# Kernel tuning notes

Hardware: AMD Instinct MI355X
Metric: run time of the kernel (lower is better)

## Reference

```python
import jax, jax.numpy as jnp
import numpy as np

B, L, H = 32, 512, 1024
Q = 128
VA_H = 256

def setup_inputs() -> dict:
    key = jax.random.key(0)
    ks = jax.random.split(key, 12)
    hidden_states = jax.random.normal(ks[0], (B, L, H), dtype=jnp.float32)
    # Build valid inclusive spans: start in [2, L-16), length in [0, 8)
    asp_s = jax.random.randint(ks[1], (B, Q), 2, L - 16)
    asp_e = asp_s + jax.random.randint(ks[2], (B, Q), 0, 8)
    opi_s = jax.random.randint(ks[3], (B, Q), 2, L - 16)
    opi_e = opi_s + jax.random.randint(ks[4], (B, Q), 0, 8)
    null = jax.random.uniform(ks[5], (B, Q)) < 0.1
    asp_s = jnp.where(null, 0, asp_s)
    quad_spans = jnp.stack([asp_s, asp_e, opi_s, opi_e], axis=-1).astype(jnp.int64)
    quad_mask = (jax.random.uniform(ks[6], (B, Q)) > 0.3).astype(jnp.float32)
    # MLP params (torch Linear: y = x @ W.T + b), kaiming-ish scale
    def lin(k, out_d, in_d):
        return jax.random.normal(k, (out_d, in_d), dtype=jnp.float32) / np.sqrt(in_d)
    W1 = lin(ks[7], VA_H, 3 * H); b1 = jnp.zeros((VA_H,), jnp.float32)
    W2 = lin(ks[8], VA_H // 2, VA_H); b2 = jnp.zeros((VA_H // 2,), jnp.float32)
    W3 = lin(ks[9], 2, VA_H // 2); b3 = jnp.zeros((2,), jnp.float32)
    return {"hidden_states": hidden_states, "quad_spans": quad_spans,
            "quad_mask": quad_mask, "W1": W1, "b1": b1, "W2": W2, "b2": b2,
            "W3": W3, "b3": b3}

def _pool_spans(hidden_states, s, e):
    # hidden_states: [B,L,H]; s,e: [B,Q] inclusive indices
    pos = jnp.arange(hidden_states.shape[1])  # [L]
    valid = (s >= 2) & (e >= s)               # [B,Q]
    m = (pos[None, None, :] >= s[..., None]) & (pos[None, None, :] <= e[..., None])
    m = (m & valid[..., None]).astype(hidden_states.dtype)  # [B,Q,L]
    cnt = jnp.maximum(m.sum(-1, keepdims=True), 1.0)        # [B,Q,1]
    mean = jnp.einsum('bql,blh->bqh', m, hidden_states) / cnt
    sep = hidden_states[:, 1:2, :]                           # [B,1,H] fallback
    return jnp.where(valid[..., None], mean, sep)

def reference(hidden_states, quad_spans, quad_mask, W1, b1, W2, b2, W3, b3):
    h_asp = _pool_spans(hidden_states, quad_spans[..., 0], quad_spans[..., 1])
    h_opi = _pool_spans(hidden_states, quad_spans[..., 2], quad_spans[..., 3])
    h_pair = jnp.concatenate([h_asp, h_opi, h_asp * h_opi], axis=-1)  # [B,Q,3H]
    x = jax.nn.gelu(h_pair @ W1.T + b1, approximate=False)  # torch GELU = erf
    x = jax.nn.gelu(x @ W2.T + b2, approximate=False)
    va = jax.nn.sigmoid(x @ W3.T + b3) * 8.0 + 1.0          # [B,Q,2] in [1,9]
    # Invalid pairs stay zero, matching the torch loop's skipped entries
    return va * (quad_mask >= 0.5).astype(va.dtype)[..., None]
```

## Files before the change

kernel.cpp:

```cpp
#include <hip/hip_runtime.h>
#include <hip/hip_bf16.h>
#include <math.h>

typedef __bf16 bf16x8 __attribute__((ext_vector_type(8)));
typedef float f32x4 __attribute__((ext_vector_type(4)));

__device__ __forceinline__ unsigned short f2bf(float x) {
    union { float f; unsigned int u; } v; v.f = x;
    unsigned int r = v.u + 0x7fffu + ((v.u >> 16) & 1u);
    return (unsigned short)(r >> 16);
}
__device__ __forceinline__ float gelu_exact(float v) {
    return 0.5f * v * (1.0f + erff(v * 0.70710678118654752f));
}

__global__ __launch_bounds__(256) void prep_kernel(const float* __restrict__ hs,
                                                   const int* __restrict__ spans,
                                                   const float* __restrict__ W1,
                                                   unsigned short* __restrict__ hp,
                                                   unsigned short* __restrict__ w1b,
                                                   float* __restrict__ xacc1) {
    const int blk = blockIdx.x;
    const int tid = threadIdx.x;

    if (blk >= 4096) {
        if (blk < 4864) {
            const int i = (blk - 4096) * 256 + tid;
            float4 f = ((const float4*)W1)[i];
            ushort4 u;
            u.x = f2bf(f.x); u.y = f2bf(f.y); u.z = f2bf(f.z); u.w = f2bf(f.w);
            ((ushort4*)w1b)[i] = u;
        } else {
            const int i = (blk - 4864) * 256 + tid;
            ((float4*)xacc1)[i] = make_float4(0.f, 0.f, 0.f, 0.f);
        }
        return;
    }

    const int pair = blk;
    const int b = pair >> 7;

    const bool is64 = (spans[1] == 0);
    int s_a, e_a, s_o, e_o;
    if (is64) {
        s_a = spans[(pair * 4 + 0) * 2]; e_a = spans[(pair * 4 + 1) * 2];
        s_o = spans[(pair * 4 + 2) * 2]; e_o = spans[(pair * 4 + 3) * 2];
    } else {
        s_a = spans[pair * 4 + 0]; e_a = spans[pair * 4 + 1];
        s_o = spans[pair * 4 + 2]; e_o = spans[pair * 4 + 3];
    }

    const float4* base = (const float4*)hs + (size_t)b * 512 * 256;

    float4 A, O;
    if (s_a >= 2 && e_a >= s_a) {
        float sx = 0.f, sy = 0.f, sz = 0.f, sw = 0.f;
        for (int t = s_a; t <= e_a; ++t) {
            float4 v = base[t * 256 + tid];
            sx += v.x; sy += v.y; sz += v.z; sw += v.w;
        }
        float inv = 1.0f / (float)(e_a - s_a + 1);
        A.x = sx * inv; A.y = sy * inv; A.z = sz * inv; A.w = sw * inv;
    } else {
        A = base[256 + tid];
    }
    if (s_o >= 2 && e_o >= s_o) {
        float sx = 0.f, sy = 0.f, sz = 0.f, sw = 0.f;
        for (int t = s_o; t <= e_o; ++t) {
            float4 v = base[t * 256 + tid];
            sx += v.x; sy += v.y; sz += v.z; sw += v.w;
        }
        float inv = 1.0f / (float)(e_o - s_o + 1);
        O.x = sx * inv; O.y = sy * inv; O.z = sz * inv; O.w = sw * inv;
    } else {
        O = base[256 + tid];
    }

    unsigned short* row = hp + (size_t)pair * 3072;
    const int d = tid * 4;
    ushort4 pa, po, pp;
    pa.x = f2bf(A.x); pa.y = f2bf(A.y); pa.z = f2bf(A.z); pa.w = f2bf(A.w);
    po.x = f2bf(O.x); po.y = f2bf(O.y); po.z = f2bf(O.z); po.w = f2bf(O.w);
    pp.x = f2bf(A.x * O.x); pp.y = f2bf(A.y * O.y);
    pp.z = f2bf(A.z * O.z); pp.w = f2bf(A.w * O.w);
    *(ushort4*)(row + d) = pa;
    *(ushort4*)(row + 1024 + d) = po;
    *(ushort4*)(row + 2048 + d) = pp;
}

__global__ __launch_bounds__(256, 4) void gemm1_mfma(const unsigned short* __restrict__ A,
                                                     const unsigned short* __restrict__ Bw,
                                                     float* __restrict__ xacc) {
    __shared__ __align__(16) unsigned short As[128 * 64];
    __shared__ __align__(16) unsigned short Bs[64 * 64];

    const int tid = threadIdx.x;
    const int lane = tid & 63;
    const int wid = tid >> 6;
    const int quad = lane >> 4;
    const int l16 = lane & 15;
    const int wM = wid * 32;
    const int m0 = blockIdx.x * 128;
    const int n0 = blockIdx.y * 64;
    const int kb = blockIdx.z * 384;

    const int srow = tid >> 3;
    const int lchunk = (tid & 7) ^ (srow & 7);
    const unsigned short* Abase = A + (size_t)(m0 + srow) * 3072 + kb + lchunk * 8;
    const unsigned short* Bbase = Bw + (size_t)(n0 + srow) * 3072 + kb + lchunk * 8;

    int aoff[2][2], boff[4][2];
#pragma unroll
    for (int h = 0; h < 2; ++h) {
#pragma unroll
        for (int mi = 0; mi < 2; ++mi) {
            const int row = wM + mi * 16 + l16;
            const int pc = (h * 4 + quad) ^ (row & 7);
            aoff[mi][h] = row * 64 + pc * 8;
        }
#pragma unroll
        for (int ni = 0; ni < 4; ++ni) {
            const int row = ni * 16 + l16;
            const int pc = (h * 4 + quad) ^ (row & 7);
            boff[ni][h] = row * 64 + pc * 8;
        }
    }

    f32x4 acc[2][4] = {};

#pragma unroll
    for (int it = 0; it < 6; ++it) {
        const int kadv = it * 64;
#pragma unroll
        for (int j = 0; j < 4; ++j) {
            __builtin_amdgcn_global_load_lds(
                (const __attribute__((address_space(1))) void*)(Abase + (size_t)j * 32 * 3072 + kadv),
                (__attribute__((address_space(3))) void*)(&As[(j * 256 + tid) * 8]),
                16, 0, 0);
        }
#pragma unroll
        for (int j = 0; j < 2; ++j) {
            __builtin_amdgcn_global_load_lds(
                (const __attribute__((address_space(1))) void*)(Bbase + (size_t)j * 32 * 3072 + kadv),
                (__attribute__((address_space(3))) void*)(&Bs[(j * 256 + tid) * 8]),
                16, 0, 0);
        }
        __syncthreads();
#pragma unroll
        for (int h = 0; h < 2; ++h) {
            bf16x8 af[2], bfr[4];
#pragma unroll
            for (int mi = 0; mi < 2; ++mi) af[mi] = *(const bf16x8*)&As[aoff[mi][h]];
#pragma unroll
            for (int ni = 0; ni < 4; ++ni) bfr[ni] = *(const bf16x8*)&Bs[boff[ni][h]];
#pragma unroll
            for (int mi = 0; mi < 2; ++mi)
#pragma unroll
                for (int ni = 0; ni < 4; ++ni)
                    acc[mi][ni] = __builtin_amdgcn_mfma_f32_16x16x32_bf16(
                        af[mi], bfr[ni], acc[mi][ni], 0, 0, 0);
        }
        __syncthreads();
    }

#pragma unroll
    for (int mi = 0; mi < 2; ++mi) {
#pragma unroll
        for (int ni = 0; ni < 4; ++ni) {
            const int n = n0 + ni * 16 + l16;
#pragma unroll
            for (int rr = 0; rr < 4; ++rr) {
                const int m = m0 + wM + mi * 16 + quad * 4 + rr;
                unsafeAtomicAdd(&xacc[(size_t)m * 256 + n], acc[mi][ni][rr]);
            }
        }
    }
}

__global__ __launch_bounds__(256) void mlp2g_head(const float* __restrict__ xacc,
                                                  const float* __restrict__ b1,
                                                  const float* __restrict__ W2f,
                                                  const float* __restrict__ b2,
                                                  const float* __restrict__ W3,
                                                  const float* __restrict__ b3,
                                                  const float* __restrict__ mask,
                                                  float* __restrict__ out) {
    __shared__ __align__(16) unsigned short Xs[32][72];
    __shared__ __align__(16) unsigned short Ws[128][72];
    __shared__ float X2[32][132];

    const int tid = threadIdx.x;
    const int lane = tid & 63;
    const int wid = tid >> 6;
    const int wM = (wid >> 1) * 16;
    const int wN = (wid & 1) * 64;
    const int quad = lane >> 4;
    const int l16 = lane & 15;
    const int m0 = blockIdx.x * 32;

    f32x4 acc[4] = {};

    for (int k0 = 0; k0 < 256; k0 += 64) {
        {
            const int r = tid >> 3, c = (tid & 7) * 8;
            const float* src = xacc + (size_t)(m0 + r) * 256 + k0 + c;
            float4 f0 = *(const float4*)src;
            float4 f1 = *(const float4*)(src + 4);
            float4 g0 = *(const float4*)(b1 + k0 + c);
            float4 g1 = *(const float4*)(b1 + k0 + c + 4);
            ushort4 u0, u1;
            u0.x = f2bf(gelu_exact(f0.x + g0.x)); u0.y = f2bf(gelu_exact(f0.y + g0.y));
            u0.z = f2bf(gelu_exact(f0.z + g0.z)); u0.w = f2bf(gelu_exact(f0.w + g0.w));
            u1.x = f2bf(gelu_exact(f1.x + g1.x)); u1.y = f2bf(gelu_exact(f1.y + g1.y));
            u1.z = f2bf(gelu_exact(f1.z + g1.z)); u1.w = f2bf(gelu_exact(f1.w + g1.w));
            *(ushort4*)&Xs[r][c] = u0;
            *(ushort4*)&Xs[r][c + 4] = u1;
        }
#pragma unroll
        for (int p = 0; p < 4; ++p) {
            const int v = tid + p * 256;
            const int r = v >> 3, c = (v & 7) * 8;
            const float* src = W2f + (size_t)r * 256 + k0 + c;
            float4 f0 = *(const float4*)src;
            float4 f1 = *(const float4*)(src + 4);
            ushort4 u;
            u.x = f2bf(f0.x); u.y = f2bf(f0.y); u.z = f2bf(f0.z); u.w = f2bf(f0.w);
            *(ushort4*)&Ws[r][c] = u;
            u.x = f2bf(f1.x); u.y = f2bf(f1.y); u.z = f2bf(f1.z); u.w = f2bf(f1.w);
            *(ushort4*)&Ws[r][c + 4] = u;
        }
        __syncthreads();
#pragma unroll
        for (int kk = 0; kk < 64; kk += 32) {
            bf16x8 a = *(const bf16x8*)&Xs[wM + l16][kk + quad * 8];
#pragma unroll
            for (int ni = 0; ni < 4; ++ni) {
                bf16x8 b = *(const bf16x8*)&Ws[wN + ni * 16 + l16][kk + quad * 8];
                acc[ni] = __builtin_amdgcn_mfma_f32_16x16x32_bf16(a, b, acc[ni], 0, 0, 0);
            }
        }
        __syncthreads();
    }

#pragma unroll
    for (int ni = 0; ni < 4; ++ni) {
        const int n = wN + ni * 16 + l16;
        const float bn = b2[n];
#pragma unroll
        for (int rr = 0; rr < 4; ++rr) {
            const int m = wM + quad * 4 + rr;
            X2[m][n] = gelu_exact(acc[ni][rr] + bn);
        }
    }
    __syncthreads();

    const int p = tid >> 3;
    const int cc = (tid & 7) * 16;
    float a0 = 0.f, a1 = 0.f;
#pragma unroll
    for (int j = 0; j < 16; ++j) {
        const float xv = X2[p][cc + j];
        a0 += xv * W3[cc + j];
        a1 += xv * W3[128 + cc + j];
    }
    a0 += __shfl_xor(a0, 1); a0 += __shfl_xor(a0, 2); a0 += __shfl_xor(a0, 4);
    a1 += __shfl_xor(a1, 1); a1 += __shfl_xor(a1, 2); a1 += __shfl_xor(a1, 4);
    if ((tid & 7) == 0) {
        const int pair = m0 + p;
        const float mk = (mask[pair] >= 0.5f) ? 1.0f : 0.0f;
        out[pair * 2 + 0] = ((1.0f / (1.0f + expf(-(a0 + b3[0])))) * 8.0f + 1.0f) * mk;
        out[pair * 2 + 1] = ((1.0f / (1.0f + expf(-(a1 + b3[1])))) * 8.0f + 1.0f) * mk;
    }
}

extern "C" void kernel_launch(void* const* d_in, const int* in_sizes, int n_in,
                              void* d_out, int out_size, void* d_ws, size_t ws_size,
                              hipStream_t stream) {
    const float* hs   = (const float*)d_in[0];
    const int*   spans= (const int*)d_in[1];
    const float* mask = (const float*)d_in[2];
    const float* W1   = (const float*)d_in[3];
    const float* b1   = (const float*)d_in[4];
    const float* W2   = (const float*)d_in[5];
    const float* b2   = (const float*)d_in[6];
    const float* W3   = (const float*)d_in[7];
    const float* b3   = (const float*)d_in[8];
    float* out = (float*)d_out;

    unsigned short* hp    = (unsigned short*)d_ws;
    float*          xacc1 = (float*)((char*)d_ws + 25165824);
    unsigned short* w1b   = (unsigned short*)((char*)d_ws + 29360128);

    prep_kernel<<<dim3(5888), dim3(256), 0, stream>>>(hs, spans, W1, hp, w1b, xacc1);
    gemm1_mfma<<<dim3(32, 4, 8), dim3(256), 0, stream>>>(hp, w1b, xacc1);
    mlp2g_head<<<dim3(128), dim3(256), 0, stream>>>(xacc1, b1, W2, b2, W3, b3, mask, out);
}
```

Baseline: 161.3 us.

## Fuse GEMM1, MLP layer 2 and head into one double-buffered kernel

Replaces the split-K GEMM1 with its atomic accumulation buffer, and the separate MLP2/head kernel, with a single kernel. Each block owns 16 rows and computes all 256 hidden columns over the full K=3072, using double-buffered LDS tiles. GELU, layer 2 and the head then run on-chip, which removes the xacc zeroing, the atomics and one launch. The cost is only 256 blocks, each streaming the whole W1 (about 1.5MB) through a single K loop. That gives lower parallelism and a much larger total W1 read volume, mostly served from L2.

```diff
diff --git a/kernel.cpp b/kernel.cpp
--- a/kernel.cpp
+++ b/kernel.cpp
@@ -10,6 +10,10 @@
     unsigned int r = v.u + 0x7fffu + ((v.u >> 16) & 1u);
     return (unsigned short)(r >> 16);
 }
+__device__ __forceinline__ float bf2f(unsigned short h) {
+    union { unsigned int u; float f; } v; v.u = ((unsigned int)h) << 16;
+    return v.f;
+}
 __device__ __forceinline__ float gelu_exact(float v) {
     return 0.5f * v * (1.0f + erff(v * 0.70710678118654752f));
 }
@@ -18,22 +22,16 @@
                                                    const int* __restrict__ spans,
                                                    const float* __restrict__ W1,
                                                    unsigned short* __restrict__ hp,
-                                                   unsigned short* __restrict__ w1b,
-                                                   float* __restrict__ xacc1) {
+                                                   unsigned short* __restrict__ w1b) {
     const int blk = blockIdx.x;
     const int tid = threadIdx.x;
 
     if (blk >= 4096) {
-        if (blk < 4864) {
-            const int i = (blk - 4096) * 256 + tid;
-            float4 f = ((const float4*)W1)[i];
-            ushort4 u;
-            u.x = f2bf(f.x); u.y = f2bf(f.y); u.z = f2bf(f.z); u.w = f2bf(f.w);
-            ((ushort4*)w1b)[i] = u;
-        } else {
-            const int i = (blk - 4864) * 256 + tid;
-            ((float4*)xacc1)[i] = make_float4(0.f, 0.f, 0.f, 0.f);
-        }
+        const int i = (blk - 4096) * 256 + tid;
+        float4 f = ((const float4*)W1)[i];
+        ushort4 u;
+        u.x = f2bf(f.x); u.y = f2bf(f.y); u.z = f2bf(f.z); u.w = f2bf(f.w);
+        ((ushort4*)w1b)[i] = u;
         return;
     }
 
@@ -88,184 +86,160 @@
     *(ushort4*)(row + 2048 + d) = pp;
 }
 
-__global__ __launch_bounds__(256, 4) void gemm1_mfma(const unsigned short* __restrict__ A,
-                                                     const unsigned short* __restrict__ Bw,
-                                                     float* __restrict__ xacc) {
-    __shared__ __align__(16) unsigned short As[128 * 64];
-    __shared__ __align__(16) unsigned short Bs[64 * 64];
+__global__ __launch_bounds__(256) void mlp_all(const unsigned short* __restrict__ hp,
+                                               const unsigned short* __restrict__ w1b,
+                                               const float* __restrict__ b1,
+                                               const float* __restrict__ W2f,
+                                               const float* __restrict__ b2,
+                                               const float* __restrict__ W3,
+                                               const float* __restrict__ b3,
+                                               const float* __restrict__ mask,
+                                               float* __restrict__ out) {
+    __shared__ __align__(16) unsigned char smem[84480];
+    unsigned short* Ab0 = (unsigned short*)smem;
+    unsigned short* Ab1 = (unsigned short*)(smem + 2048);
+    unsigned short* Bb0 = (unsigned short*)(smem + 4096);
+    unsigned short* Bb1 = (unsigned short*)(smem + 36864);
+    unsigned short* x1s = (unsigned short*)smem;
+    unsigned short* w2s = (unsigned short*)(smem + 8448);
+    float*          x2s = (float*)(smem + 76032);
 
     const int tid = threadIdx.x;
     const int lane = tid & 63;
     const int wid = tid >> 6;
     const int quad = lane >> 4;
     const int l16 = lane & 15;
-    const int wM = wid * 32;
-    const int m0 = blockIdx.x * 128;
-    const int n0 = blockIdx.y * 64;
-    const int kb = blockIdx.z * 384;
+    const int m0 = blockIdx.x * 16;
 
     const int srow = tid >> 3;
-    const int lchunk = (tid & 7) ^ (srow & 7);
-    const unsigned short* Abase = A + (size_t)(m0 + srow) * 3072 + kb + lchunk * 8;
-    const unsigned short* Bbase = Bw + (size_t)(n0 + srow) * 3072 + kb + lchunk * 8;
-
-    int aoff[2][2], boff[4][2];
+    const int lch = (tid & 7) ^ (srow & 7);
+    const unsigned short* Aptr = hp + (size_t)(m0 + srow) * 3072 + lch * 8;
+    const unsigned short* Bptr = w1b + (size_t)srow * 3072 + lch * 8;
+
+    int aoff[2], boff[4][2];
 #pragma unroll
     for (int h = 0; h < 2; ++h) {
-#pragma unroll
-        for (int mi = 0; mi < 2; ++mi) {
-            const int row = wM + mi * 16 + l16;
-            const int pc = (h * 4 + quad) ^ (row & 7);
-            aoff[mi][h] = row * 64 + pc * 8;
+        {
+            const int pc = (h * 4 + quad) ^ (l16 & 7);
+            aoff[h] = l16 * 64 + pc * 8;
         }
 #pragma unroll
         for (int ni = 0; ni < 4; ++ni) {
-            const int row = ni * 16 + l16;
+            const int row = wid * 64 + ni * 16 + l16;
             const int pc = (h * 4 + quad) ^ (row & 7);
             boff[ni][h] = row * 64 + pc * 8;
         }
     }
 
-    f32x4 acc[2][4] = {};
-
-#pragma unroll
-    for (int it = 0; it < 6; ++it) {
-        const int kadv = it * 64;
-#pragma unroll
-        for (int j = 0; j < 4; ++j) {
-            __builtin_amdgcn_global_load_lds(
-                (const __attribute__((address_space(1))) void*)(Abase + (size_t)j * 32 * 3072 + kadv),
-                (__attribute__((address_space(3))) void*)(&As[(j * 256 + tid) * 8]),
-                16, 0, 0);
-        }
-#pragma unroll
-        for (int j = 0; j < 2; ++j) {
-            __builtin_amdgcn_global_load_lds(
-                (const __attribute__((address_space(1))) void*)(Bbase + (size_t)j * 32 * 3072 + kadv),
-                (__attribute__((address_space(3))) void*)(&Bs[(j * 256 + tid) * 8]),
-                16, 0, 0);
-        }
+    f32x4 acc[4] = {};
+
+    if (tid < 128)
+        __builtin_amdgcn_global_load_lds(
+            (const __attribute__((address_space(1))) void*)Aptr,
+            (__attribute__((address_space(3))) void*)(Ab0 + tid * 8), 16, 0, 0);
+#pragma unroll
+    for (int j = 0; j < 8; ++j)
+        __builtin_amdgcn_global_load_lds(
+            (const __attribute__((address_space(1))) void*)(Bptr + (size_t)j * 32 * 3072),
+            (__attribute__((address_space(3))) void*)(Bb0 + (j * 256 + tid) * 8), 16, 0, 0);
+
+    for (int it = 0; it < 48; ++it) {
+        unsigned short* Ac = (it & 1) ? Ab1 : Ab0;
+        unsigned short* Bc = (it & 1) ? Bb1 : Bb0;
         __syncthreads();
+        if (it + 1 < 48) {
+            unsigned short* An = (it & 1) ? Ab0 : Ab1;
+            unsigned short* Bn = (it & 1) ? Bb0 : Bb1;
+            const int kadv = (it + 1) * 64;
+            if (tid < 128)
+                __builtin_amdgcn_global_load_lds(
+                    (const __attribute__((address_space(1))) void*)(Aptr + kadv),
+                    (__attribute__((address_space(3))) void*)(An + tid * 8), 16, 0, 0);
+#pragma unroll
+            for (int j = 0; j < 8; ++j)
+                __builtin_amdgcn_global_load_lds(
+                    (const __attribute__((address_space(1))) void*)(Bptr + (size_t)j * 32 * 3072 + kadv),
+                    (__attribute__((address_space(3))) void*)(Bn + (j * 256 + tid) * 8), 16, 0, 0);
+        }
 #pragma unroll
         for (int h = 0; h < 2; ++h) {
-            bf16x8 af[2], bfr[4];
-#pragma unroll
-            for (int mi = 0; mi < 2; ++mi) af[mi] = *(const bf16x8*)&As[aoff[mi][h]];
-#pragma unroll
-            for (int ni = 0; ni < 4; ++ni) bfr[ni] = *(const bf16x8*)&Bs[boff[ni][h]];
-#pragma unroll
-            for (int mi = 0; mi < 2; ++mi)
-#pragma unroll
-                for (int ni = 0; ni < 4; ++ni)
-                    acc[mi][ni] = __builtin_amdgcn_mfma_f32_16x16x32_bf16(
-                        af[mi], bfr[ni], acc[mi][ni], 0, 0, 0);
-        }
-        __syncthreads();
-    }
-
-#pragma unroll
-    for (int mi = 0; mi < 2; ++mi) {
-#pragma unroll
-        for (int ni = 0; ni < 4; ++ni) {
-            const int n = n0 + ni * 16 + l16;
-#pragma unroll
-            for (int rr = 0; rr < 4; ++rr) {
-                const int m = m0 + wM + mi * 16 + quad * 4 + rr;
-                unsafeAtomicAdd(&xacc[(size_t)m * 256 + n], acc[mi][ni][rr]);
-            }
-        }
-    }
-}
-
-__global__ __launch_bounds__(256) void mlp2g_head(const float* __restrict__ xacc,
-                                                  const float* __restrict__ b1,
-                                                  const float* __restrict__ W2f,
-                                                  const float* __restrict__ b2,
-                                                  const float* __restrict__ W3,
-                                                  const float* __restrict__ b3,
-                                                  const float* __restrict__ mask,
-                                                  float* __restrict__ out) {
-    __shared__ __align__(16) unsigned short Xs[32][72];
-    __shared__ __align__(16) unsigned short Ws[128][72];
-    __shared__ float X2[32][132];
-
-    const int tid = threadIdx.x;
-    const int lane = tid & 63;
-    const int wid = tid >> 6;
-    const int wM = (wid >> 1) * 16;
-    const int wN = (wid & 1) * 64;
-    const int quad = lane >> 4;
-    const int l16 = lane & 15;
-    const int m0 = blockIdx.x * 32;
-
-    f32x4 acc[4] = {};
-
-    for (int k0 = 0; k0 < 256; k0 += 64) {
-        {
-            const int r = tid >> 3, c = (tid & 7) * 8;
-            const float* src = xacc + (size_t)(m0 + r) * 256 + k0 + c;
-            float4 f0 = *(const float4*)src;
-            float4 f1 = *(const float4*)(src + 4);
-            float4 g0 = *(const float4*)(b1 + k0 + c);
-            float4 g1 = *(const float4*)(b1 + k0 + c + 4);
-            ushort4 u0, u1;
-            u0.x = f2bf(gelu_exact(f0.x + g0.x)); u0.y = f2bf(gelu_exact(f0.y + g0.y));
-            u0.z = f2bf(gelu_exact(f0.z + g0.z)); u0.w = f2bf(gelu_exact(f0.w + g0.w));
-            u1.x = f2bf(gelu_exact(f1.x + g1.x)); u1.y = f2bf(gelu_exact(f1.y + g1.y));
-            u1.z = f2bf(gelu_exact(f1.z + g1.z)); u1.w = f2bf(gelu_exact(f1.w + g1.w));
-            *(ushort4*)&Xs[r][c] = u0;
-            *(ushort4*)&Xs[r][c + 4] = u1;
-        }
-#pragma unroll
-        for (int p = 0; p < 4; ++p) {
-            const int v = tid + p * 256;
-            const int r = v >> 3, c = (v & 7) * 8;
-            const float* src = W2f + (size_t)r * 256 + k0 + c;
-            float4 f0 = *(const float4*)src;
-            float4 f1 = *(const float4*)(src + 4);
-            ushort4 u;
-            u.x = f2bf(f0.x); u.y = f2bf(f0.y); u.z = f2bf(f0.z); u.w = f2bf(f0.w);
-            *(ushort4*)&Ws[r][c] = u;
-            u.x = f2bf(f1.x); u.y = f2bf(f1.y); u.z = f2bf(f1.z); u.w = f2bf(f1.w);
-            *(ushort4*)&Ws[r][c + 4] = u;
-        }
-        __syncthreads();
-#pragma unroll
-        for (int kk = 0; kk < 64; kk += 32) {
-            bf16x8 a = *(const bf16x8*)&Xs[wM + l16][kk + quad * 8];
+            bf16x8 a = *(const bf16x8*)&Ac[aoff[h]];
 #pragma unroll
             for (int ni = 0; ni < 4; ++ni) {
-                bf16x8 b = *(const bf16x8*)&Ws[wN + ni * 16 + l16][kk + quad * 8];
+                bf16x8 b = *(const bf16x8*)&Bc[boff[ni][h]];
                 acc[ni] = __builtin_amdgcn_mfma_f32_16x16x32_bf16(a, b, acc[ni], 0, 0, 0);
             }
         }
-        __syncthreads();
-    }
+    }
+
+    __syncthreads();
 
 #pragma unroll
     for (int ni = 0; ni < 4; ++ni) {
-        const int n = wN + ni * 16 + l16;
-        const float bn = b2[n];
+        const int col = wid * 64 + ni * 16 + l16;
+        const float bn = b1[col];
 #pragma unroll
         for (int rr = 0; rr < 4; ++rr) {
-            const int m = wM + quad * 4 + rr;
-            X2[m][n] = gelu_exact(acc[ni][rr] + bn);
-        }
+            const int row = quad * 4 + rr;
+            x1s[row * 264 + col] = f2bf(gelu_exact(acc[ni][rr] + bn));
+        }
+    }
+#pragma unroll
+    for (int p = 0; p < 16; ++p) {
+        const int v = p * 256 + tid;
+        const int r = v >> 5;
+        const int c = (v & 31) * 8;
+        const float* src = W2f + (size_t)r * 256 + c;
+        float4 f0 = *(const float4*)src;
+        float4 f1 = *(const float4*)(src + 4);
+        ushort4 u0, u1;
+        u0.x = f2bf(f0.x); u0.y = f2bf(f0.y); u0.z = f2bf(f0.z); u0.w = f2bf(f0.w);
+        u1.x = f2bf(f1.x); u1.y = f2bf(f1.y); u1.z = f2bf(f1.z); u1.w = f2bf(f1.w);
+        *(ushort4*)&w2s[r * 264 + c] = u0;
+        *(ushort4*)&w2s[r * 264 + c + 4] = u1;
     }
     __syncthreads();
 
-    const int p = tid >> 3;
-    const int cc = (tid & 7) * 16;
+    f32x4 acc2[2] = {};
+#pragma unroll
+    for (int h2 = 0; h2 < 8; ++h2) {
+        const int k = h2 * 32 + quad * 8;
+        bf16x8 a = *(const bf16x8*)&x1s[l16 * 264 + k];
+#pragma unroll
+        for (int ni = 0; ni < 2; ++ni) {
+            const int r = wid * 32 + ni * 16 + l16;
+            bf16x8 b = *(const bf16x8*)&w2s[r * 264 + k];
+            acc2[ni] = __builtin_amdgcn_mfma_f32_16x16x32_bf16(a, b, acc2[ni], 0, 0, 0);
+        }
+    }
+
+#pragma unroll
+    for (int ni = 0; ni < 2; ++ni) {
+        const int col = wid * 32 + ni * 16 + l16;
+        const float bn = b2[col];
+#pragma unroll
+        for (int rr = 0; rr < 4; ++rr) {
+            const int row = quad * 4 + rr;
+            x2s[row * 132 + col] = gelu_exact(acc2[ni][rr] + bn);
+        }
+    }
+    __syncthreads();
+
+    const int p = tid >> 4;
+    const int cg = tid & 15;
+    const int c0 = cg * 8;
     float a0 = 0.f, a1 = 0.f;
 #pragma unroll
-    for (int j = 0; j < 16; ++j) {
-        const float xv = X2[p][cc + j];
-        a0 += xv * W3[cc + j];
-        a1 += xv * W3[128 + cc + j];
-    }
-    a0 += __shfl_xor(a0, 1); a0 += __shfl_xor(a0, 2); a0 += __shfl_xor(a0, 4);
-    a1 += __shfl_xor(a1, 1); a1 += __shfl_xor(a1, 2); a1 += __shfl_xor(a1, 4);
-    if ((tid & 7) == 0) {
+    for (int j = 0; j < 8; ++j) {
+        const float xv = x2s[p * 132 + c0 + j];
+        a0 += xv * W3[c0 + j];
+        a1 += xv * W3[128 + c0 + j];
+    }
+    a0 += __shfl_xor(a0, 1); a0 += __shfl_xor(a0, 2);
+    a0 += __shfl_xor(a0, 4); a0 += __shfl_xor(a0, 8);
+    a1 += __shfl_xor(a1, 1); a1 += __shfl_xor(a1, 2);
+    a1 += __shfl_xor(a1, 4); a1 += __shfl_xor(a1, 8);
+    if (cg == 0) {
         const int pair = m0 + p;
         const float mk = (mask[pair] >= 0.5f) ? 1.0f : 0.0f;
         out[pair * 2 + 0] = ((1.0f / (1.0f + expf(-(a0 + b3[0])))) * 8.0f + 1.0f) * mk;
@@ -287,11 +261,9 @@
     const float* b3   = (const float*)d_in[8];
     float* out = (float*)d_out;
 
-    unsigned short* hp    = (unsigned short*)d_ws;
-    float*          xacc1 = (float*)((char*)d_ws + 25165824);
-    unsigned short* w1b   = (unsigned short*)((char*)d_ws + 29360128);
-
-    prep_kernel<<<dim3(5888), dim3(256), 0, stream>>>(hs, spans, W1, hp, w1b, xacc1);
-    gemm1_mfma<<<dim3(32, 4, 8), dim3(256), 0, stream>>>(hp, w1b, xacc1);
-    mlp2g_head<<<dim3(128), dim3(256), 0, stream>>>(xacc1, b1, W2, b2, W3, b3, mask, out);
-}
+    unsigned short* hp  = (unsigned short*)d_ws;
+    unsigned short* w1b = (unsigned short*)((char*)d_ws + 25165824);
+
+    prep_kernel<<<dim3(4864), dim3(256), 0, stream>>>(hs, spans, W1, hp, w1b);
+    mlp_all<<<dim3(256), dim3(256), 0, stream>>>(hp, w1b, b1, W2, b2, W3, b3, mask, out);
+}
```

Result: no change. 158.6 us (-1.6%).
